# Kernel tuning notes

Measured on AMD Instinct MI355X. Metric: run time of the kernel, lower is better.

## Reference

```python
import jax, jax.numpy as jnp
import numpy as np

S = 4          # num_segments
T = 4096       # frames
D = 1024       # input_size == output_size
HEADS = 1
FREQ = 10000.0
DH = D // HEADS     # per-head width = 1024
TB = T // S         # block height = 1024
WB = DH // S        # block width  = 256


def _abs_pos(tb, d, freq):
    # Matches getAbsolutePosition: AP[p, 2i] = sin(p / freq^(2i/d)), AP[p, 2i+1] = cos(same).
    pos = jnp.arange(tb, dtype=jnp.float32)[:, None]          # [tb,1]
    i = jnp.arange(tb // 2, dtype=jnp.float32)[None, :]       # [1,tb//2]
    ang = pos / jnp.power(jnp.float32(freq), 2.0 * i / d)     # [tb,tb//2]
    ap = jnp.zeros((tb, tb), jnp.float32)
    return ap.at[:, 0::2].set(jnp.sin(ang)).at[:, 1::2].set(jnp.cos(ang))


def setup_inputs() -> dict:
    key = jax.random.key(0)
    ks = jax.random.split(key, 6)
    x = jax.random.normal(ks[0], (T, D), jnp.float32)
    Wq = jax.random.normal(ks[1], (HEADS, DH, D), jnp.float32) * 0.02
    Wk = jax.random.normal(ks[2], (HEADS, DH, D), jnp.float32) * 0.02
    Wv = jax.random.normal(ks[3], (HEADS, DH, D), jnp.float32) * 0.02
    Wout = jax.random.normal(ks[4], (D, D), jnp.float32) * 0.02
    Wout2 = jax.random.normal(ks[5], (WB, WB + 2), jnp.float32) * 0.05
    return {"x": x, "Wq": Wq, "Wk": Wk, "Wv": Wv, "Wout": Wout, "Wout2": Wout2}


def _forward(x, Wq, Wk, Wv, Wout, Wout2):
    # diversity = 1 - cosine similarity (F.normalize p=2 along dim=1)
    xu = x / jnp.maximum(jnp.linalg.norm(x, axis=1, keepdims=True), 1e-12)
    div = 1.0 - xu @ xu.T                                     # [T,T]

    Q = jnp.einsum('ti,hdi->htd', x, Wq)                      # [h,T,DH]
    K = jnp.einsum('ti,hdi->htd', x, Wk)
    V = jnp.einsum('ti,hdi->htd', x, Wv)

    def blk(A):  # [h,T,DH] -> [h,S*S,TB,WB], block (i,j) row-major as in local_x/local_y
        return A.reshape(-1, S, TB, S, WB).transpose(0, 1, 3, 2, 4).reshape(-1, S * S, TB, WB)

    qb, kb, vb = blk(Q), blk(K), blk(V)
    # diversity uses the diagonal row-block for every column-block j of row i
    drow = jnp.stack([div[i * TB:(i + 1) * TB, i * TB:(i + 1) * TB] for i in range(S)], 0)  # [S,TB,TB]
    db = jnp.repeat(drow, S, axis=0)[None]                    # [1,S*S,TB,TB]

    sim = jnp.einsum('hbqc,hbkc->hbqk', qb, kb) + _abs_pos(TB, D, FREQ)  # [h,S*S,TB,TB]
    attw = jax.nn.softmax(sim, axis=-1)
    # normalized row entropy, then L1-normalized (F.normalize p=1)
    ent = -(attw * jax.nn.log_softmax(sim, axis=-1)).sum(-1) / jnp.log(jnp.float32(TB))  # [h,S*S,TB]
    ent = ent / jnp.maximum(jnp.abs(ent).sum(-1, keepdims=True), 1e-12)

    dep = (db * attw).sum(-1) / db.sum(-1)                    # [h,S*S,TB]
    att_win = attw + dep[:, :, None, :] * attw                # dep_factor rows are identical
    ctx = jnp.einsum('hbqk,hbkc->hbqc', att_win, vb)          # [h,S*S,TB,WB]

    chars = jax.lax.stop_gradient(jnp.stack([ent, dep], axis=-1))  # [h,S*S,TB,2] (detach)
    y = jnp.concatenate([ctx, chars], axis=-1) @ Wout2.T      # [h,S*S,TB,WB]

    # reassemble grid of blocks back to [h,T,DH], concat heads, final projection
    y = y.reshape(-1, S, S, TB, WB).transpose(0, 1, 3, 2, 4).reshape(-1, T, DH)
    y = y.transpose(1, 0, 2).reshape(T, HEADS * DH)
    return y @ Wout.T                                         # [T,D]


def reference(x, Wq, Wk, Wv, Wout, Wout2):
    return _forward(x, Wq, Wk, Wv, Wout, Wout2)
```

## Files before the change

### kernel.cpp

```cpp
#include <hip/hip_runtime.h>
#include <hip/hip_bf16.h>

#define TT 4096
#define DD 1024
#define TBB 1024
#define WBB 256

typedef __attribute__((ext_vector_type(8))) _Float16 half8;
typedef __attribute__((ext_vector_type(4))) _Float16 half4;
typedef __attribute__((ext_vector_type(16))) float f32x16;

__device__ __forceinline__ unsigned short f2h(float v) {
  _Float16 h = (_Float16)v;
  return *reinterpret_cast<unsigned short*>(&h);
}
__device__ __forceinline__ float h2f(unsigned short u) {
  _Float16 h = *reinterpret_cast<_Float16*>(&u);
  return (float)h;
}

__device__ __forceinline__ void gl_lds16(const unsigned short* g, unsigned short* l) {
  __builtin_amdgcn_global_load_lds(
      (const __attribute__((address_space(1))) void*)(unsigned long long)(g),
      (__attribute__((address_space(3))) void*)(unsigned long long)(l),
      16, 0, 0);
}

__device__ __forceinline__ float waveSum(float v) {
#pragma unroll
  for (int o = 32; o > 0; o >>= 1) v += __shfl_down(v, o, 64);
  return v;
}
__device__ __forceinline__ float bSum(float v) {
#pragma unroll
  for (int o = 32; o > 0; o >>= 1) v += __shfl_xor(v, o, 64);
  return v;
}
__device__ __forceinline__ float bMax(float v) {
#pragma unroll
  for (int o = 32; o > 0; o >>= 1) v = fmaxf(v, __shfl_xor(v, o, 64));
  return v;
}

template <int EPI, typename OutT>
__device__ __forceinline__ void g64_body(
    const unsigned short* __restrict__ Ab, const unsigned short* __restrict__ Bb,
    OutT* __restrict__ Cb, int K, int lda, int ldb, int ldc,
    int bx, int by,
    const float* __restrict__ e0, const float* __restrict__ e1,
    const float* __restrict__ e2, const float* __restrict__ e3,
    unsigned short* __restrict__ lA, unsigned short* __restrict__ lB)
{
  const int m0 = by * 64, n0 = bx * 64;
  const int tid = threadIdx.x, wave = tid >> 6, lane = tid & 63;
  const int wm = (wave >> 1) * 32, wn = (wave & 1) * 32;
  const int srow = lane >> 2;
  const int grow = wave * 16 + srow;
  const int scol = (((lane & 3) ^ ((grow >> 1) & 3))) * 8;
  const int l31 = lane & 31, khi = lane >> 5;
  const int sw2 = (l31 >> 1) & 3;

  f32x16 acc = {};

  for (int k0 = 0; k0 < K; k0 += 64) {
#pragma unroll
    for (int h = 0; h < 2; ++h) {
      gl_lds16(Ab + (long)(m0 + grow) * lda + (k0 + h * 32 + scol), &lA[h * 2048 + wave * 512]);
      gl_lds16(Bb + (long)(n0 + grow) * ldb + (k0 + h * 32 + scol), &lB[h * 2048 + wave * 512]);
    }
    __syncthreads();

    half8 af[4], bfr[4];
#pragma unroll
    for (int ks = 0; ks < 4; ++ks) {
      af[ks] = *(const half8*)&lA[(ks >> 1) * 2048 + (wm + l31) * 32 + ((((ks & 1) * 2 + khi) ^ sw2) * 8)];
      bfr[ks] = *(const half8*)&lB[(ks >> 1) * 2048 + (wn + l31) * 32 + ((((ks & 1) * 2 + khi) ^ sw2) * 8)];
    }
#pragma unroll
    for (int ks = 0; ks < 4; ++ks)
      acc = __builtin_amdgcn_mfma_f32_32x32x16_f16(af[ks], bfr[ks], acc, 0, 0, 0);
    __syncthreads();
  }

  float Ef[4], Df[4];
  if constexpr (EPI == 4) {
    const int col0 = n0 + wn + l31;
#pragma unroll
    for (int j = 0; j < 4; ++j) {
      Ef[j] = e2[j * 1024 + col0];
      Df[j] = e3[j * 1024 + col0];
    }
  }
#pragma unroll
  for (int r = 0; r < 16; ++r) {
    const int row = m0 + wm + khi * 4 + (r & 3) + 8 * (r >> 2);
    const int col = n0 + wn + l31;
    float v = acc[r];
    if constexpr (EPI == 1 || EPI == 2) v = 1.0f - v;
    if constexpr (EPI == 4) {
      const float4 en = *(const float4*)(e0 + (long)row * 4);
      const float4 dp = *(const float4*)(e1 + (long)row * 4);
      v += en.x * Ef[0] + en.y * Ef[1] + en.z * Ef[2] + en.w * Ef[3]
         + dp.x * Df[0] + dp.y * Df[1] + dp.z * Df[2] + dp.w * Df[3];
    }
    const long ci = (long)row * ldc + col;
    if constexpr (sizeof(OutT) == 2) {
      Cb[ci] = (OutT)f2h(v);
    } else {
      Cb[ci] = v;
    }
  }

  if constexpr (EPI == 2) {
    if (bx != by) {
      unsigned short* mir = lA;
      const int lc = wn + l31;
#pragma unroll
      for (int chunk = 0; chunk < 2; ++chunk) {
        __syncthreads();
        if ((lc >> 5) == chunk) {
#pragma unroll
          for (int r = 0; r < 16; ++r) {
            const int lr = wm + khi * 4 + (r & 3) + 8 * (r >> 2);
            mir[(lc & 31) * 68 + lr] = f2h(1.0f - acc[r]);
          }
        }
        __syncthreads();
        const int cl = tid >> 3, co = (tid & 7) * 8;
        const ushort4 a = *(const ushort4*)&mir[cl * 68 + co];
        const ushort4 b = *(const ushort4*)&mir[cl * 68 + co + 4];
        unsigned short* dst = (unsigned short*)Cb + (long)(n0 + chunk * 32 + cl) * ldc + m0 + co;
        *(ushort4*)dst = a;
        *(ushort4*)(dst + 4) = b;
      }
    }
  }
}

__device__ __forceinline__ void g128_body(
    const unsigned short* __restrict__ Ab, const unsigned short* __restrict__ Bb,
    unsigned short* __restrict__ Cb, int K, int lda, int ldb, int ldc,
    int bx, int by,
    unsigned short* __restrict__ lA, unsigned short* __restrict__ lB)
{
  const int m0 = by * 128, n0 = bx * 128;
  const int tid = threadIdx.x, wave = tid >> 6, lane = tid & 63;
  const int wm = (wave >> 1) * 64, wn = (wave & 1) * 64;
  const int srow = lane >> 2;
  const int scol = (((lane & 3) ^ ((srow >> 1) & 3))) * 8;
  const int l31 = lane & 31, khi = lane >> 5;
  const int sw2 = (l31 >> 1) & 3;

  f32x16 acc[2][2] = {};

  for (int k0 = 0; k0 < K; k0 += 64) {
#pragma unroll
    for (int h = 0; h < 2; ++h)
#pragma unroll
      for (int t = 0; t < 2; ++t) {
        const int r = wave * 32 + t * 16 + srow;
        gl_lds16(Ab + (long)(m0 + r) * lda + (k0 + h * 32 + scol), &lA[h * 4096 + wave * 1024 + t * 512]);
        gl_lds16(Bb + (long)(n0 + r) * ldb + (k0 + h * 32 + scol), &lB[h * 4096 + wave * 1024 + t * 512]);
      }
    __syncthreads();

    half8 af[2][4], bfr[2][4];
#pragma unroll
    for (int mi = 0; mi < 2; ++mi)
#pragma unroll
      for (int ks = 0; ks < 4; ++ks)
        af[mi][ks] = *(const half8*)&lA[(ks >> 1) * 4096 + (wm + mi * 32 + l31) * 32 + ((((ks & 1) * 2 + khi) ^ sw2) * 8)];
#pragma unroll
    for (int ni = 0; ni < 2; ++ni)
#pragma unroll
      for (int ks = 0; ks < 4; ++ks)
        bfr[ni][ks] = *(const half8*)&lB[(ks >> 1) * 4096 + (wn + ni * 32 + l31) * 32 + ((((ks & 1) * 2 + khi) ^ sw2) * 8)];

#pragma unroll
    for (int ks = 0; ks < 4; ++ks)
#pragma unroll
      for (int mi = 0; mi < 2; ++mi)
#pragma unroll
        for (int ni = 0; ni < 2; ++ni)
          acc[mi][ni] = __builtin_amdgcn_mfma_f32_32x32x16_f16(af[mi][ks], bfr[ni][ks], acc[mi][ni], 0, 0, 0);
    __syncthreads();
  }

#pragma unroll
  for (int mi = 0; mi < 2; ++mi)
#pragma unroll
    for (int ni = 0; ni < 2; ++ni)
#pragma unroll
      for (int r = 0; r < 16; ++r) {
        const int row = m0 + wm + mi * 32 + khi * 4 + (r & 3) + 8 * (r >> 2);
        const int col = n0 + wn + ni * 32 + l31;
        Cb[(long)row * ldc + col] = f2h(acc[mi][ni][r]);
      }
}

template <int EPI, typename OutT>
__global__ __launch_bounds__(256) void gemm_s(
    const unsigned short* __restrict__ A, const unsigned short* __restrict__ B,
    OutT* __restrict__ C,
    int K, int lda, int ldb, int ldc,
    int zbase, int zdiv,
    long sAi, long sAj, long sBi, long sBj, long sCi, long sCj,
    long sAz, long sBz, long sCz,
    const float* __restrict__ e0, const float* __restrict__ e1,
    const float* __restrict__ e2, const float* __restrict__ e3)
{
  __shared__ __align__(16) unsigned short lA[2 * 2048];
  __shared__ __align__(16) unsigned short lB[2 * 2048];

  if constexpr (EPI == 2) {
    if (blockIdx.x < blockIdx.y) return;
  }
  const int z = blockIdx.z, gz = zbase + z;
  const int zi = gz / zdiv, zj = gz - zi * zdiv;
  const unsigned short* Ab = A + (long)zi * sAi + (long)zj * sAj + (long)z * sAz;
  const unsigned short* Bb = B + (long)zi * sBi + (long)zj * sBj + (long)z * sBz;
  OutT* Cb = C + (long)zi * sCi + (long)zj * sCj + (long)z * sCz;
  g64_body<EPI, OutT>(Ab, Bb, Cb, K, lda, ldb, ldc, blockIdx.x, blockIdx.y,
                      e0, e1, e2, e3, lA, lB);
}

__global__ __launch_bounds__(256) void mega1_kernel(
    const unsigned short* __restrict__ xh, const unsigned short* __restrict__ Wh,
    unsigned short* __restrict__ QKV,
    unsigned short* __restrict__ Vt,
    const unsigned short* __restrict__ xu, unsigned short* __restrict__ divb,
    const unsigned short* __restrict__ WoB, const unsigned short* __restrict__ W2T,
    unsigned short* __restrict__ WFh)
{
  __shared__ __align__(16) unsigned short lbuf[16384];

  int b = blockIdx.x;
  if (b < 512) {
    const int z = b >> 8, rem = b & 255, by = rem >> 3, bx = rem & 7;
    g128_body(xh, Wh + (long)z * DD * DD, QKV + (long)z * TT * DD,
              DD, DD, DD, DD, bx, by, lbuf, lbuf + 8192);
    return;
  }
  b -= 512;
  if (b < 1024) {
    const int bx = b & 63, by = b >> 6;
    g64_body<0, unsigned short>(Wh + (size_t)2 * DD * DD, xh, Vt, DD, DD, DD, TT, bx, by,
                                nullptr, nullptr, nullptr, nullptr, lbuf, lbuf + 4096);
    return;
  }
  b -= 1024;
  if (b < 1024) {
    const int z = b >> 8, r = b & 255, bx = r & 15, by = r >> 4;
    if (bx < by) return;
    const unsigned short* Xu = xu + (long)z * TBB * DD;
    g64_body<2, unsigned short>(Xu, Xu, divb + (long)z * TBB * TBB,
                                DD, DD, DD, TBB, bx, by,
                                nullptr, nullptr, nullptr, nullptr, lbuf, lbuf + 4096);
    return;
  }
  b -= 1024;
  {
    const int zj = b >> 6, r = b & 63, bx = r & 3, by = r >> 2;
    g64_body<0, unsigned short>(WoB + zj * 256, W2T, WFh + zj * 256,
                                256, DD, 256, DD, bx, by,
                                nullptr, nullptr, nullptr, nullptr, lbuf, lbuf + 4096);
  }
}

__global__ __launch_bounds__(256) void sim_gemm(
    const unsigned short* __restrict__ A, const unsigned short* __restrict__ B,
    unsigned short* __restrict__ C,
    const unsigned short* __restrict__ APh)
{
  __shared__ __align__(16) unsigned short lA[2][4096];
  __shared__ __align__(16) unsigned short lB[2][4096];

  const int gz = blockIdx.z;
  const int zi = gz >> 2, zj = gz & 3;
  const unsigned short* Ab = A + (long)zi * (TBB * DD) + zj * WBB;
  const unsigned short* Bb = B + (long)zi * (TBB * DD) + zj * WBB;
  unsigned short* Cb = C + (long)gz * TBB * TBB;

  const int m0 = blockIdx.y * 128, n0 = blockIdx.x * 128;
  const int tid = threadIdx.x, wave = tid >> 6, lane = tid & 63;
  const int wm = (wave >> 1) * 64, wn = (wave & 1) * 64;
  const int srow = lane >> 2;
  const int scol = ((lane & 3) ^ ((srow >> 1) & 3)) * 8;
  const int l31 = lane & 31, khi = lane >> 5;
  const int sw2 = (l31 >> 1) & 3;

  f32x16 acc[2][2] = {};

  for (int k0 = 0; k0 < WBB; k0 += 64) {
#pragma unroll
    for (int h = 0; h < 2; ++h)
#pragma unroll
      for (int t = 0; t < 2; ++t) {
        const int r = wave * 32 + t * 16 + srow;
        gl_lds16(Ab + (long)(m0 + r) * DD + (k0 + h * 32 + scol), &lA[h][wave * 1024 + t * 512]);
        gl_lds16(Bb + (long)(n0 + r) * DD + (k0 + h * 32 + scol), &lB[h][wave * 1024 + t * 512]);
      }
    __syncthreads();

    half8 af[2][4], bfr[2][4];
#pragma unroll
    for (int mi = 0; mi < 2; ++mi)
#pragma unroll
      for (int ks = 0; ks < 4; ++ks)
        af[mi][ks] = *(const half8*)&lA[ks >> 1][(wm + mi * 32 + l31) * 32 + ((((ks & 1) * 2 + khi) ^ sw2) * 8)];
#pragma unroll
    for (int ni = 0; ni < 2; ++ni)
#pragma unroll
      for (int ks = 0; ks < 4; ++ks)
        bfr[ni][ks] = *(const half8*)&lB[ks >> 1][(wn + ni * 32 + l31) * 32 + ((((ks & 1) * 2 + khi) ^ sw2) * 8)];

#pragma unroll
    for (int ks = 0; ks < 4; ++ks)
#pragma unroll
      for (int mi = 0; mi < 2; ++mi)
#pragma unroll
        for (int ni = 0; ni < 2; ++ni)
          acc[mi][ni] = __builtin_amdgcn_mfma_f32_32x32x16_f16(af[mi][ks], bfr[ni][ks], acc[mi][ni], 0, 0, 0);
    __syncthreads();
  }

#pragma unroll
  for (int mi = 0; mi < 2; ++mi)
#pragma unroll
    for (int ni = 0; ni < 2; ++ni)
#pragma unroll
      for (int r = 0; r < 16; ++r) {
        const int row = m0 + wm + mi * 32 + khi * 4 + (r & 3) + 8 * (r >> 2);
        const int col = n0 + wn + ni * 32 + l31;
        Cb[(long)row * TBB + col] = f2h(acc[mi][ni][r] + h2f(APh[(long)row * 1024 + col]));
      }
}

__global__ __launch_bounds__(256) void ctx_gemm_s(
    const unsigned short* __restrict__ simh, const float* __restrict__ dep2,
    const float* __restrict__ Brow,
    const unsigned short* __restrict__ Vt, unsigned short* __restrict__ ctxR,
    float* __restrict__ ent2)
{
  const int tid = threadIdx.x;

  if (blockIdx.y == 16) {
    if (blockIdx.x != 0 || blockIdx.z >= 4) return;
    const int b = blockIdx.z;
    float4 v[4];
    float4 a = {0.f, 0.f, 0.f, 0.f};
#pragma unroll
    for (int p = 0; p < 4; ++p) {
      v[p] = *(const float4*)(ent2 + ((long)b * 1024 + tid + p * 256) * 4);
      a.x += fabsf(v[p].x); a.y += fabsf(v[p].y);
      a.z += fabsf(v[p].z); a.w += fabsf(v[p].w);
    }
    a.x = waveSum(a.x); a.y = waveSum(a.y);
    a.z = waveSum(a.z); a.w = waveSum(a.w);
    __shared__ float red[4][4];
    if ((tid & 63) == 0) {
      const int w = tid >> 6;
      red[w][0] = a.x; red[w][1] = a.y; red[w][2] = a.z; red[w][3] = a.w;
    }
    __syncthreads();
    float4 sc;
    sc.x = 1.f / fmaxf(red[0][0] + red[1][0] + red[2][0] + red[3][0], 1e-12f);
    sc.y = 1.f / fmaxf(red[0][1] + red[1][1] + red[2][1] + red[3][1], 1e-12f);
    sc.z = 1.f / fmaxf(red[0][2] + red[1][2] + red[2][2] + red[3][2], 1e-12f);
    sc.w = 1.f / fmaxf(red[0][3] + red[1][3] + red[2][3] + red[3][3], 1e-12f);
#pragma unroll
    for (int p = 0; p < 4; ++p) {
      float4 o = v[p];
      o.x *= sc.x; o.y *= sc.y; o.z *= sc.z; o.w *= sc.w;
      *(float4*)(ent2 + ((long)b * 1024 + tid + p * 256) * 4) = o;
    }
    return;
  }

  __shared__ __align__(16) unsigned short lA[2][2048];
  __shared__ __align__(16) unsigned short lB[2][4096];
  __shared__ __align__(16) unsigned short sDepH[1024];

  const int gz = blockIdx.z, zi = gz >> 2, zj = gz & 3;
  const int m0 = blockIdx.y * 64, n0 = blockIdx.x * 128;
  const int wave = tid >> 6, lane = tid & 63;
  const int wm = (wave >> 1) * 32, wn0 = (wave & 1) * 64;
  const int srow = lane >> 2;
  const int grow = wave * 16 + srow;
  const int scol = ((lane & 3) ^ ((grow >> 1) & 3)) * 8;
  const int l31 = lane & 31, khi = lane >> 5;
  const int sw2 = (l31 >> 1) & 3;

#pragma unroll
  for (int p = 0; p < 4; ++p)
    sDepH[tid + p * 256] =
        f2h(1.f + dep2[((long)zi * 1024 + tid + p * 256) * 4 + zj]);
  __syncthreads();

  const float B0 = Brow[(long)gz * 1024 + m0 + (tid >> 3)];
  const float B1 = Brow[(long)gz * 1024 + m0 + 32 + (tid >> 3)];

  const unsigned short* Ab = simh + (long)gz * TBB * TBB;
  const unsigned short* Bb = Vt + (long)(zj * 256) * TT + (long)zi * 1024;

  f32x16 acc[2] = {};

  for (int k0 = 0; k0 < 1024; k0 += 64) {
#pragma unroll
    for (int h = 0; h < 2; ++h) {
      gl_lds16(Bb + (long)(n0 + grow) * TT + (k0 + h * 32 + scol), &lB[h][wave * 512]);
      gl_lds16(Bb + (long)(n0 + 64 + grow) * TT + (k0 + h * 32 + scol), &lB[h][2048 + wave * 512]);
    }
#pragma unroll
    for (int h = 0; h < 2; ++h)
#pragma unroll
      for (int p = 0; p < 2; ++p) {
        const int idx = p * 1024 + tid * 4;
        const int row = idx >> 5, col = idx & 31;
        const ushort4 wv = *(const ushort4*)(Ab + (long)(m0 + row) * 1024 + k0 + h * 32 + col);
        const float Bp = p ? B1 : B0;
        half4 ev;
        ev.x = (_Float16)exp2f(fmaf(h2f(wv.x), 1.4426950408889634f, -Bp));
        ev.y = (_Float16)exp2f(fmaf(h2f(wv.y), 1.4426950408889634f, -Bp));
        ev.z = (_Float16)exp2f(fmaf(h2f(wv.z), 1.4426950408889634f, -Bp));
        ev.w = (_Float16)exp2f(fmaf(h2f(wv.w), 1.4426950408889634f, -Bp));
        const half4 dv = *(const half4*)&sDepH[k0 + h * 32 + col];
        half4 pv = ev * dv;
        const int pcol = (((col >> 3) ^ ((row >> 1) & 3)) << 3) | (col & 7);
        *(half4*)&lA[h][row * 32 + pcol] = pv;
      }
    __syncthreads();

    half8 af[4], bfr[2][4];
#pragma unroll
    for (int ks = 0; ks < 4; ++ks) {
      af[ks] = *(const half8*)&lA[ks >> 1][(wm + l31) * 32 + ((((ks & 1) * 2 + khi) ^ sw2) * 8)];
#pragma unroll
      for (int n = 0; n < 2; ++n)
        bfr[n][ks] = *(const half8*)&lB[ks >> 1][(wn0 + n * 32 + l31) * 32 + ((((ks & 1) * 2 + khi) ^ sw2) * 8)];
    }
#pragma unroll
    for (int ks = 0; ks < 4; ++ks)
#pragma unroll
      for (int n = 0; n < 2; ++n)
        acc[n] = __builtin_amdgcn_mfma_f32_32x32x16_f16(af[ks], bfr[n][ks], acc[n], 0, 0, 0);
    __syncthreads();
  }

#pragma unroll
  for (int n = 0; n < 2; ++n)
#pragma unroll
    for (int r = 0; r < 16; ++r) {
      const int row = m0 + wm + khi * 4 + (r & 3) + 8 * (r >> 2);
      const int col = n0 + wn0 + n * 32 + l31;
      ctxR[((long)zi * 1024 + row) * 1024 + zj * 256 + col] = f2h(acc[n][r]);
    }
}

__global__ __launch_bounds__(256) void prep_kernel(
    const float* __restrict__ x, const float* __restrict__ Wq,
    const float* __restrict__ Wk, const float* __restrict__ Wv,
    const float* __restrict__ Wo, const float* __restrict__ W2,
    unsigned short* __restrict__ xh, unsigned short* __restrict__ xu,
    unsigned short* __restrict__ Wh, unsigned short* __restrict__ APh,
    unsigned short* __restrict__ WoB, unsigned short* __restrict__ W2T,
    float* __restrict__ Efold, float* __restrict__ Dfold)
{
  __shared__ float red[4];
  int b = blockIdx.x;
  const int tid = threadIdx.x;

  if (b < 4096) {
    const int t = b;
    const float4 v = *((const float4*)(x + (long)t * DD) + tid);
    float ss = v.x * v.x + v.y * v.y + v.z * v.z + v.w * v.w;
    ss = waveSum(ss);
    if ((tid & 63) == 0) red[tid >> 6] = ss;
    __syncthreads();
    const float tot = red[0] + red[1] + red[2] + red[3];
    const float inv = 1.f / fmaxf(sqrtf(tot), 1e-12f);
    ushort4 h, u;
    h.x = f2h(v.x); h.y = f2h(v.y); h.z = f2h(v.z); h.w = f2h(v.w);
    u.x = f2h(v.x * inv); u.y = f2h(v.y * inv); u.z = f2h(v.z * inv); u.w = f2h(v.w * inv);
    *((ushort4*)(xh + (long)t * DD) + tid) = h;
    *((ushort4*)(xu + (long)t * DD) + tid) = u;
    return;
  }
  b -= 4096;
  if (b < 3072) {
    const long idx4 = ((long)b * 256 + tid) * 4;
    const int which = (int)(idx4 >> 20);
    const long loc = idx4 & ((1L << 20) - 1);
    const float* src = (which == 0) ? Wq : ((which == 1) ? Wk : Wv);
    const float4 v = *(const float4*)(src + loc);
    ushort4 h;
    h.x = f2h(v.x); h.y = f2h(v.y); h.z = f2h(v.z); h.w = f2h(v.w);
    *(ushort4*)(Wh + idx4) = h;
    return;
  }
  b -= 3072;
  if (b < 1024) {
    const int p = b;
#pragma unroll
    for (int t = 0; t < 2; ++t) {
      const int pr = tid + t * 256;
      const float e = (float)pr * (1.0f / 512.0f);
      const float ang = (float)p * exp2f(e * -13.287712379549449f);
      float s, c;
      sincosf(ang, &s, &c);
      ushort2 o;
      o.x = f2h(s); o.y = f2h(c);
      *(ushort2*)(APh + (long)p * 1024 + 2 * pr) = o;
    }
    return;
  }
  b -= 1024;
  if (b < 1024) {
    const long idx4 = ((long)b * 256 + tid) * 4;
    const float4 v = *(const float4*)(Wo + idx4);
    ushort4 h;
    h.x = f2h(v.x); h.y = f2h(v.y); h.z = f2h(v.z); h.w = f2h(v.w);
    *(ushort4*)(WoB + idx4) = h;
    return;
  }
  b -= 1024;
  if (b < 256) {
    const int w = b;
    W2T[tid * 256 + w] = f2h(W2[w * 258 + tid]);
    return;
  }
  b -= 256;
  {
    const int wave = tid >> 6, lane = tid & 63;
    float we[4], wd[4];
#pragma unroll
    for (int u = 0; u < 4; ++u) {
      we[u] = W2[(lane * 4 + u) * 258 + 256];
      wd[u] = W2[(lane * 4 + u) * 258 + 257];
    }
    for (int i = 0; i < 16; ++i) {
      const int pidx = (b * 4 + wave) * 16 + i;
      const int j = pidx >> 10, d = pidx & 1023;
      const float4 v = *(const float4*)(Wo + (long)d * 1024 + j * 256 + lane * 4);
      float se = v.x * we[0] + v.y * we[1] + v.z * we[2] + v.w * we[3];
      float sd = v.x * wd[0] + v.y * wd[1] + v.z * wd[2] + v.w * wd[3];
      se = bSum(se);
      sd = bSum(sd);
      if (lane == 0) {
        Efold[j * 1024 + d] = se;
        Dfold[j * 1024 + d] = sd;
      }
    }
  }
}

__global__ __launch_bounds__(256) void stats_kernel(
    const unsigned short* __restrict__ sim, const unsigned short* __restrict__ divb,
    float* __restrict__ dep2, float* __restrict__ ent2,
    float* __restrict__ Brow)
{
  __shared__ __align__(16) unsigned short sDiv[1024];
  const int q = blockIdx.x, bi = blockIdx.y;
  const int tid = threadIdx.x;
  const int wave = tid >> 6, lane = tid & 63;

  *(ushort4*)&sDiv[tid * 4] =
      *(const ushort4*)(divb + ((long)bi * TBB + q) * TBB + tid * 4);
  __syncthreads();

  const int gz = bi * 4 + wave;
  const unsigned short* srow = sim + ((long)gz * TBB + q) * TBB;
  float s[16], d[16];
#pragma unroll
  for (int u = 0; u < 4; ++u) {
    const ushort4 sv = *(const ushort4*)(srow + u * 256 + lane * 4);
    const ushort4 dv = *(const ushort4*)&sDiv[u * 256 + lane * 4];
    s[u * 4 + 0] = h2f(sv.x); s[u * 4 + 1] = h2f(sv.y);
    s[u * 4 + 2] = h2f(sv.z); s[u * 4 + 3] = h2f(sv.w);
    d[u * 4 + 0] = h2f(dv.x); d[u * 4 + 1] = h2f(dv.y);
    d[u * 4 + 2] = h2f(dv.z); d[u * 4 + 3] = h2f(dv.w);
  }
  float m = s[0];
#pragma unroll
  for (int i = 1; i < 16; ++i) m = fmaxf(m, s[i]);
  m = bMax(m);
  const float mB = m * 1.4426950408889634f;
  float l = 0.f, ss = 0.f, dn = 0.f, ds = 0.f;
#pragma unroll
  for (int i = 0; i < 16; ++i) {
    const float e = exp2f(fmaf(s[i], 1.4426950408889634f, -mB));
    l += e; ss += e * s[i]; dn += e * d[i]; ds += d[i];
  }
  l = bSum(l); ss = bSum(ss); dn = bSum(dn); ds = bSum(ds);
  if (lane == 0) {
    const float Li = 1.f / l;
    const float lnL = logf(l);
    const long o2 = ((long)bi * 1024 + q) * 4 + wave;
    dep2[o2] = (dn * Li) / ds;
    ent2[o2] = (m + lnL - ss * Li) * 0.14426950408889634f;
    Brow[(long)gz * TBB + q] = (m + lnL) * 1.4426950408889634f;
  }
}

extern "C" void kernel_launch(void* const* d_in, const int* in_sizes, int n_in,
                              void* d_out, int out_size, void* d_ws, size_t ws_size,
                              hipStream_t stream)
{
  const float* x  = (const float*)d_in[0];
  const float* Wq = (const float*)d_in[1];
  const float* Wk = (const float*)d_in[2];
  const float* Wv = (const float*)d_in[3];
  const float* Wo = (const float*)d_in[4];
  const float* W2 = (const float*)d_in[5];

  char* ws = (char*)d_ws;
  size_t off = 0;
  auto take = [&](size_t bytes) -> void* {
    void* p = ws + off;
    off += (bytes + 255) & ~(size_t)255;
    return p;
  };
  unsigned short* QKV = (unsigned short*)take((size_t)2 * TT * DD * 2);
  unsigned short* xh  = (unsigned short*)take((size_t)TT * DD * 2);
  unsigned short* xu  = (unsigned short*)take((size_t)TT * DD * 2);
  unsigned short* Wh  = (unsigned short*)take((size_t)3 * DD * DD * 2);
  unsigned short* WoB = (unsigned short*)take((size_t)DD * DD * 2);
  unsigned short* W2T = (unsigned short*)take((size_t)256 * 256 * 2);
  unsigned short* WFh = (unsigned short*)take((size_t)DD * DD * 2);
  float* Efold = (float*)take((size_t)4 * DD * 4);
  float* Dfold = (float*)take((size_t)4 * DD * 4);
  unsigned short* APh = (unsigned short*)take((size_t)TBB * TBB * 2);
  unsigned short* divb = (unsigned short*)take((size_t)4 * TBB * TBB * 2);
  unsigned short* Vt = (unsigned short*)take((size_t)DD * TT * 2);
  unsigned short* simh = (unsigned short*)take((size_t)16 * TBB * TBB * 2);
  float* dep2 = (float*)take((size_t)TT * 4 * 4);
  float* ent2 = (float*)take((size_t)TT * 4 * 4);
  float* Brow = (float*)take((size_t)16 * TBB * 4);
  unsigned short* ctxR = (unsigned short*)take((size_t)TT * DD * 2);
  (void)ws_size; (void)in_sizes; (void)n_in; (void)out_size;

  prep_kernel<<<9536, 256, 0, stream>>>(x, Wq, Wk, Wv, Wo, W2,
                                        xh, xu, Wh, APh, WoB, W2T, Efold, Dfold);

  mega1_kernel<<<2816, 256, 0, stream>>>(
      xh, Wh, QKV, Vt, xu, divb, WoB, W2T, WFh);

  const unsigned short* Qh = QKV;
  const unsigned short* Kh = QKV + (size_t)TT * DD;

  sim_gemm<<<dim3(8, 8, 16), 256, 0, stream>>>(Qh, Kh, simh, APh);

  stats_kernel<<<dim3(TBB, 4), 256, 0, stream>>>(simh, divb, dep2, ent2, Brow);

  ctx_gemm_s<<<dim3(2, 17, 16), 256, 0, stream>>>(simh, dep2, Brow, Vt, ctxR, ent2);

  gemm_s<4, float><<<dim3(16, 64, 1), 256, 0, stream>>>(
      ctxR, WFh, (float*)d_out,
      DD, DD, DD, DD, 0, 1,
      0, 0, 0, 0, 0, 0,
      0, 0, 0, ent2, dep2, Efold, Dfold);
}
```

Before: 241.8 us.

## Switch mega1 sub-GEMMs to 128x128 tiles and compute full diversity blocks

The V-transpose, diversity and weight-fold GEMMs inside the fused first kernel move from 64x64 tiles to the 128x128 tile body, cutting the grid from 2816 to 1088 blocks and raising data reuse per block. The diversity GEMM no longer exploits symmetry: it computes every tile instead of the upper triangle plus an LDS-mirrored transpose store. The aim is fewer blocks and less epilogue synchronisation, at the cost of redundant diversity FLOPs. The gemm_s wrapper also drops its unused batching-stride parameters.

```diff
diff --git a/kernel.cpp b/kernel.cpp
--- a/kernel.cpp
+++ b/kernel.cpp
@@ -96,7 +96,6 @@
     const int row = m0 + wm + khi * 4 + (r & 3) + 8 * (r >> 2);
     const int col = n0 + wn + l31;
     float v = acc[r];
-    if constexpr (EPI == 1 || EPI == 2) v = 1.0f - v;
     if constexpr (EPI == 4) {
       const float4 en = *(const float4*)(e0 + (long)row * 4);
       const float4 dp = *(const float4*)(e1 + (long)row * 4);
@@ -110,33 +109,9 @@
       Cb[ci] = v;
     }
   }
-
-  if constexpr (EPI == 2) {
-    if (bx != by) {
-      unsigned short* mir = lA;
-      const int lc = wn + l31;
-#pragma unroll
-      for (int chunk = 0; chunk < 2; ++chunk) {
-        __syncthreads();
-        if ((lc >> 5) == chunk) {
-#pragma unroll
-          for (int r = 0; r < 16; ++r) {
-            const int lr = wm + khi * 4 + (r & 3) + 8 * (r >> 2);
-            mir[(lc & 31) * 68 + lr] = f2h(1.0f - acc[r]);
-          }
-        }
-        __syncthreads();
-        const int cl = tid >> 3, co = (tid & 7) * 8;
-        const ushort4 a = *(const ushort4*)&mir[cl * 68 + co];
-        const ushort4 b = *(const ushort4*)&mir[cl * 68 + co + 4];
-        unsigned short* dst = (unsigned short*)Cb + (long)(n0 + chunk * 32 + cl) * ldc + m0 + co;
-        *(ushort4*)dst = a;
-        *(ushort4*)(dst + 4) = b;
-      }
-    }
-  }
-}
-
+}
+
+template <int EPI>
 __device__ __forceinline__ void g128_body(
     const unsigned short* __restrict__ Ab, const unsigned short* __restrict__ Bb,
     unsigned short* __restrict__ Cb, int K, int lda, int ldb, int ldc,
@@ -194,7 +169,9 @@
       for (int r = 0; r < 16; ++r) {
         const int row = m0 + wm + mi * 32 + khi * 4 + (r & 3) + 8 * (r >> 2);
         const int col = n0 + wn + ni * 32 + l31;
-        Cb[(long)row * ldc + col] = f2h(acc[mi][ni][r]);
+        float v = acc[mi][ni][r];
+        if constexpr (EPI == 1) v = 1.0f - v;
+        Cb[(long)row * ldc + col] = f2h(v);
       }
 }
 
@@ -203,24 +180,12 @@
     const unsigned short* __restrict__ A, const unsigned short* __restrict__ B,
     OutT* __restrict__ C,
     int K, int lda, int ldb, int ldc,
-    int zbase, int zdiv,
-    long sAi, long sAj, long sBi, long sBj, long sCi, long sCj,
-    long sAz, long sBz, long sCz,
     const float* __restrict__ e0, const float* __restrict__ e1,
     const float* __restrict__ e2, const float* __restrict__ e3)
 {
   __shared__ __align__(16) unsigned short lA[2 * 2048];
   __shared__ __align__(16) unsigned short lB[2 * 2048];
-
-  if constexpr (EPI == 2) {
-    if (blockIdx.x < blockIdx.y) return;
-  }
-  const int z = blockIdx.z, gz = zbase + z;
-  const int zi = gz / zdiv, zj = gz - zi * zdiv;
-  const unsigned short* Ab = A + (long)zi * sAi + (long)zj * sAj + (long)z * sAz;
-  const unsigned short* Bb = B + (long)zi * sBi + (long)zj * sBj + (long)z * sBz;
-  OutT* Cb = C + (long)zi * sCi + (long)zj * sCj + (long)z * sCz;
-  g64_body<EPI, OutT>(Ab, Bb, Cb, K, lda, ldb, ldc, blockIdx.x, blockIdx.y,
+  g64_body<EPI, OutT>(A, B, C, K, lda, ldb, ldc, blockIdx.x, blockIdx.y,
                       e0, e1, e2, e3, lA, lB);
 }
 
@@ -237,33 +202,30 @@
   int b = blockIdx.x;
   if (b < 512) {
     const int z = b >> 8, rem = b & 255, by = rem >> 3, bx = rem & 7;
-    g128_body(xh, Wh + (long)z * DD * DD, QKV + (long)z * TT * DD,
-              DD, DD, DD, DD, bx, by, lbuf, lbuf + 8192);
+    g128_body<0>(xh, Wh + (long)z * DD * DD, QKV + (long)z * TT * DD,
+                 DD, DD, DD, DD, bx, by, lbuf, lbuf + 8192);
     return;
   }
   b -= 512;
-  if (b < 1024) {
-    const int bx = b & 63, by = b >> 6;
-    g64_body<0, unsigned short>(Wh + (size_t)2 * DD * DD, xh, Vt, DD, DD, DD, TT, bx, by,
-                                nullptr, nullptr, nullptr, nullptr, lbuf, lbuf + 4096);
-    return;
-  }
-  b -= 1024;
-  if (b < 1024) {
-    const int z = b >> 8, r = b & 255, bx = r & 15, by = r >> 4;
-    if (bx < by) return;
+  if (b < 256) {
+    const int by = b >> 5, bx = b & 31;
+    g128_body<0>(Wh + (size_t)2 * DD * DD, xh, Vt, DD, DD, DD, TT, bx, by,
+                 lbuf, lbuf + 8192);
+    return;
+  }
+  b -= 256;
+  if (b < 256) {
+    const int z = b >> 6, r = b & 63, by = r >> 3, bx = r & 7;
     const unsigned short* Xu = xu + (long)z * TBB * DD;
-    g64_body<2, unsigned short>(Xu, Xu, divb + (long)z * TBB * TBB,
-                                DD, DD, DD, TBB, bx, by,
-                                nullptr, nullptr, nullptr, nullptr, lbuf, lbuf + 4096);
-    return;
-  }
-  b -= 1024;
+    g128_body<1>(Xu, Xu, divb + (long)z * TBB * TBB,
+                 DD, DD, DD, TBB, bx, by, lbuf, lbuf + 8192);
+    return;
+  }
+  b -= 256;
   {
-    const int zj = b >> 6, r = b & 63, bx = r & 3, by = r >> 2;
-    g64_body<0, unsigned short>(WoB + zj * 256, W2T, WFh + zj * 256,
-                                256, DD, 256, DD, bx, by,
-                                nullptr, nullptr, nullptr, nullptr, lbuf, lbuf + 4096);
+    const int zj = b >> 4, r = b & 15, by = r >> 1, bx = r & 1;
+    g128_body<0>(WoB + zj * 256, W2T, WFh + zj * 256,
+                 256, DD, 256, DD, bx, by, lbuf, lbuf + 8192);
   }
 }
 
@@ -642,7 +604,7 @@
   prep_kernel<<<9536, 256, 0, stream>>>(x, Wq, Wk, Wv, Wo, W2,
                                         xh, xu, Wh, APh, WoB, W2T, Efold, Dfold);
 
-  mega1_kernel<<<2816, 256, 0, stream>>>(
+  mega1_kernel<<<1088, 256, 0, stream>>>(
       xh, Wh, QKV, Vt, xu, divb, WoB, W2T, WFh);
 
   const unsigned short* Qh = QKV;
@@ -656,7 +618,6 @@
 
   gemm_s<4, float><<<dim3(16, 64, 1), 256, 0, stream>>>(
       ctxR, WFh, (float*)d_out,
-      DD, DD, DD, DD, 0, 1,
-      0, 0, 0, 0, 0, 0,
-      0, 0, 0, ent2, dep2, Efold, Dfold);
-}
+      DD, DD, DD, DD,
+      ent2, dep2, Efold, Dfold);
+}
```

After: 225.2 us. -6.9%, faster.
